# Kernel tuning notes

Hardware: AMD Instinct MI355X
Metric: run time of the kernel (lower is better)

## Reference

```python
import jax, jax.numpy as jnp
import numpy as np

K = 20
EPS = 1e-5
SLOPE = 0.2


def _leaky(v):
    return jnp.where(v >= 0, v, SLOPE * v)


def _instnorm(v, axes):
    # InstanceNorm with affine=False: normalize per (batch, channel) over spatial axes,
    # biased variance, eps=1e-5 (torch default).
    mean = jnp.mean(v, axis=axes, keepdims=True)
    var = jnp.mean((v - mean) ** 2, axis=axes, keepdims=True)
    return (v - mean) * jax.lax.rsqrt(var + EPS)


def _knn_idx(x, k):
    # x: [B, C, N]; returns indices of k nearest neighbors (self included), [B, N, k]
    inner = -2.0 * jnp.einsum('bcn,bcm->bnm', x, x)
    xx = jnp.sum(x * x, axis=1)                      # [B, N]
    pd = -xx[:, :, None] - inner - xx[:, None, :]    # negative squared distance
    return jax.lax.top_k(pd, k)[1]


def _edge_conv(x, w):
    # x: [B, C, N]; w: [O, 2C]. Returns [B, O, N] after max-pool over k neighbors.
    B, C, N = x.shape
    idx = _knn_idx(x, K)                              # [B, N, K]
    xt = jnp.transpose(x, (0, 2, 1))                  # [B, N, C]
    b_idx = jnp.arange(B)[:, None, None]
    nb = xt[b_idx, idx]                               # [B, N, K, C] gathered neighbors
    ctr = xt[:, :, None, :]                           # [B, N, 1, C]
    feat = jnp.concatenate([nb - ctr, jnp.broadcast_to(ctr, nb.shape)], axis=-1)
    h = jnp.einsum('oc,bnkc->bonk', w, feat)          # 1x1 conv as GEMM -> [B, O, N, K]
    h = _leaky(_instnorm(h, (2, 3)))
    return jnp.max(h, axis=-1)                        # [B, O, N]


def setup_inputs() -> dict:
    key = jax.random.key(0)
    ks = jax.random.split(key, 6)
    B, N, feat_dim = 8, 2048, 512
    return {
        'x': jax.random.normal(ks[0], (B, N, 3), dtype=jnp.float32),
        'w1': jax.random.normal(ks[1], (64, 6), dtype=jnp.float32) * 0.1,
        'w2': jax.random.normal(ks[2], (64, 128), dtype=jnp.float32) * 0.1,
        'w3': jax.random.normal(ks[3], (128, 128), dtype=jnp.float32) * 0.1,
        'w4': jax.random.normal(ks[4], (256, 256), dtype=jnp.float32) * 0.1,
        'w5': jax.random.normal(ks[5], (feat_dim, 512), dtype=jnp.float32) * 0.1,
    }


def reference(x, w1, w2, w3, w4, w5):
    xc = jnp.transpose(x, (0, 2, 1))                  # [B, 3, N]
    x1 = _edge_conv(xc, w1)                           # [B, 64, N]
    x2 = _edge_conv(x1, w2)                           # [B, 64, N]
    x3 = _edge_conv(x2, w3)                           # [B, 128, N]
    x4 = _edge_conv(x3, w4)                           # [B, 256, N]
    cat = jnp.concatenate([x1, x2, x3, x4], axis=1)   # [B, 512, N]
    h = jnp.einsum('oc,bcn->bon', w5, cat)            # conv5 (1x1 conv1d)
    feat = _leaky(_instnorm(h, (2,)))
    return feat                                       # [B, feat_dim, N]
```

## Files before the change

kernel.cpp:

```cpp
#include <hip/hip_runtime.h>
#include <math.h>

#define NPTS 2048
#define NB 8
#define KNN 20
#define EPSI 1e-5f
#define SLOPE 0.2f
#define CHUNK 512

__global__ __launch_bounds__(256) void transpose_kernel(const float* __restrict__ xin,
                                                        float* __restrict__ xc) {
    int g = blockIdx.x * 256 + threadIdx.x;
    int b = g / NPTS, n = g % NPTS;
    float v0 = xin[(size_t)g * 3 + 0];
    float v1 = xin[(size_t)g * 3 + 1];
    float v2 = xin[(size_t)g * 3 + 2];
    xc[((size_t)b * 3 + 0) * NPTS + n] = v0;
    xc[((size_t)b * 3 + 1) * NPTS + n] = v1;
    xc[((size_t)b * 3 + 2) * NPTS + n] = v2;
}

__global__ __launch_bounds__(256) void xx_kernel(const float* __restrict__ x, int bstride, int C,
                                                 float* __restrict__ xx) {
    int g = blockIdx.x * 256 + threadIdx.x;
    int b = g / NPTS, n = g % NPTS;
    const float* p = x + (size_t)b * bstride + n;
    float s = 0.f;
    for (int c = 0; c < C; ++c) { float v = p[(size_t)c * NPTS]; s += v * v; }
    xx[g] = s;
}

__global__ __launch_bounds__(256) void pd_gemm(const float* __restrict__ x, int bstride, int C,
                                               const float* __restrict__ xx,
                                               float* __restrict__ pd, int r0) {
    __shared__ float As[16][64];
    __shared__ float Bs[16][64];
    int b = blockIdx.z;
    int nbase_l = blockIdx.y * 64;
    int mbase = blockIdx.x * 64;
    int tx = threadIdx.x, ty = threadIdx.y;
    int tid = ty * 16 + tx;
    float acc[4][4] = {};
    const float* xb = x + (size_t)b * bstride;

    for (int c0 = 0; c0 < C; c0 += 16) {
        int KC = min(16, C - c0);
        for (int t = tid; t < KC * 64; t += 256) {
            int cc = t >> 6, j = t & 63;
            As[cc][j] = xb[(size_t)(c0 + cc) * NPTS + r0 + nbase_l + j];
            Bs[cc][j] = xb[(size_t)(c0 + cc) * NPTS + mbase + j];
        }
        __syncthreads();
        if (KC == 16) {
            #pragma unroll
            for (int cc = 0; cc < 16; ++cc) {
                float a0 = As[cc][ty*4+0], a1 = As[cc][ty*4+1], a2 = As[cc][ty*4+2], a3 = As[cc][ty*4+3];
                float b0 = Bs[cc][tx*4+0], b1 = Bs[cc][tx*4+1], b2 = Bs[cc][tx*4+2], b3 = Bs[cc][tx*4+3];
                acc[0][0] += a0*b0; acc[0][1] += a0*b1; acc[0][2] += a0*b2; acc[0][3] += a0*b3;
                acc[1][0] += a1*b0; acc[1][1] += a1*b1; acc[1][2] += a1*b2; acc[1][3] += a1*b3;
                acc[2][0] += a2*b0; acc[2][1] += a2*b1; acc[2][2] += a2*b2; acc[2][3] += a2*b3;
                acc[3][0] += a3*b0; acc[3][1] += a3*b1; acc[3][2] += a3*b2; acc[3][3] += a3*b3;
            }
        } else {
            for (int cc = 0; cc < KC; ++cc) {
                float a0 = As[cc][ty*4+0], a1 = As[cc][ty*4+1], a2 = As[cc][ty*4+2], a3 = As[cc][ty*4+3];
                float b0 = Bs[cc][tx*4+0], b1 = Bs[cc][tx*4+1], b2 = Bs[cc][tx*4+2], b3 = Bs[cc][tx*4+3];
                acc[0][0] += a0*b0; acc[0][1] += a0*b1; acc[0][2] += a0*b2; acc[0][3] += a0*b3;
                acc[1][0] += a1*b0; acc[1][1] += a1*b1; acc[1][2] += a1*b2; acc[1][3] += a1*b3;
                acc[2][0] += a2*b0; acc[2][1] += a2*b1; acc[2][2] += a2*b2; acc[2][3] += a2*b3;
                acc[3][0] += a3*b0; acc[3][1] += a3*b1; acc[3][2] += a3*b2; acc[3][3] += a3*b3;
            }
        }
        __syncthreads();
    }

    const float* xxb = xx + (size_t)b * NPTS;
    #pragma unroll
    for (int i = 0; i < 4; ++i) {
        int nl = nbase_l + ty * 4 + i;
        float xn = xxb[r0 + nl];
        float4 o;
        o.x = 2.f * acc[i][0] - xn - xxb[mbase + tx*4 + 0];
        o.y = 2.f * acc[i][1] - xn - xxb[mbase + tx*4 + 1];
        o.z = 2.f * acc[i][2] - xn - xxb[mbase + tx*4 + 2];
        o.w = 2.f * acc[i][3] - xn - xxb[mbase + tx*4 + 3];
        *(float4*)&pd[((size_t)b * CHUNK + nl) * NPTS + mbase + tx*4] = o;
    }
}

__global__ __launch_bounds__(256) void topk_kernel(const float* __restrict__ pd,
                                                   int* __restrict__ idxout, int r0) {
    int wid = (blockIdx.x * 256 + threadIdx.x) >> 6;
    int lane = threadIdx.x & 63;
    int b = wid / CHUNK;
    int nl = wid % CHUNK;
    int n = r0 + nl;
    const float* row = pd + ((size_t)b * CHUNK + nl) * NPTS;

    float v[32];
    #pragma unroll
    for (int j = 0; j < 32; ++j) v[j] = row[lane + 64 * j];

    unsigned mask = 0u;
    int saved = 0;
    for (int t = 0; t < KNN; ++t) {
        float best = -INFINITY; int bj = 0;
        #pragma unroll
        for (int j = 0; j < 32; ++j) {
            bool ok = ((mask >> j) & 1u) == 0u;
            if (ok && v[j] > best) { best = v[j]; bj = j; }
        }
        int midx = lane + 64 * bj;
        #pragma unroll
        for (int off = 32; off > 0; off >>= 1) {
            float ov = __shfl_xor(best, off);
            int om = __shfl_xor(midx, off);
            if (ov > best || (ov == best && om < midx)) { best = ov; midx = om; }
        }
        if (lane == t) saved = midx;
        if ((midx & 63) == lane) mask |= 1u << (midx >> 6);
    }
    if (lane < KNN) idxout[((size_t)b * NPTS + n) * KNN + lane] = saved;
}

__global__ __launch_bounds__(256) void yz_gemm(const float* __restrict__ x, int bstride, int C, int O,
                                               const float* __restrict__ w,
                                               float* __restrict__ y, float* __restrict__ z) {
    __shared__ float Xs[128 * 64];
    __shared__ float Ws[4 * 256];
    int b = blockIdx.z;
    int mbase = blockIdx.x * 64;
    int obase = blockIdx.y * 4;
    int tx = threadIdx.x, ty = threadIdx.y;
    int tid = ty * 64 + tx;
    const float* xb = x + (size_t)b * bstride;

    for (int t = tid; t < C * 64; t += 256) {
        int cc = t >> 6, j = t & 63;
        Xs[cc * 64 + j] = xb[(size_t)cc * NPTS + mbase + j];
    }
    int C2 = 2 * C;
    for (int t = tid; t < 4 * C2; t += 256) {
        int ol = t / C2, c = t % C2;
        Ws[ol * C2 + c] = w[(size_t)(obase + ol) * C2 + c];
    }
    __syncthreads();

    int o = obase + ty;
    const float* wr = &Ws[ty * C2];
    float ya = 0.f, za = 0.f;
    for (int c = 0; c < C; ++c) {
        float v = Xs[c * 64 + tx];
        float wd = wr[c], wc = wr[C + c];
        ya += wd * v;
        za += (wc - wd) * v;
    }
    y[((size_t)b * O + o) * NPTS + mbase + tx] = ya;
    z[((size_t)b * O + o) * NPTS + mbase + tx] = za;
}

__global__ __launch_bounds__(256) void gather_norm(const float* __restrict__ y,
                                                   const float* __restrict__ z,
                                                   const int* __restrict__ idx,
                                                   float* __restrict__ cat, int coff, int O) {
    __shared__ float yrow[NPTS];
    __shared__ float red[8];
    int o = blockIdx.x, b = blockIdx.y;
    int tid = threadIdx.x;
    const float* yr = y + ((size_t)b * O + o) * NPTS;
    for (int i = tid; i < NPTS / 4; i += 256)
        ((float4*)yrow)[i] = ((const float4*)yr)[i];
    __syncthreads();

    const float* zr = z + ((size_t)b * O + o) * NPTS;
    float s1 = 0.f, s2 = 0.f;
    float hm[8];
    #pragma unroll
    for (int r = 0; r < 8; ++r) {
        int n = r * 256 + tid;
        float zv = zr[n];
        const int* ip = idx + ((size_t)b * NPTS + n) * KNN;
        float mx = -INFINITY;
        #pragma unroll
        for (int k = 0; k < KNN; ++k) {
            float h = yrow[ip[k]] + zv;
            s1 += h; s2 += h * h;
            mx = fmaxf(mx, h);
        }
        hm[r] = mx;
    }
    #pragma unroll
    for (int off = 32; off > 0; off >>= 1) {
        s1 += __shfl_xor(s1, off);
        s2 += __shfl_xor(s2, off);
    }
    int wv = tid >> 6, lane = tid & 63;
    if (lane == 0) { red[wv] = s1; red[4 + wv] = s2; }
    __syncthreads();
    float S1 = red[0] + red[1] + red[2] + red[3];
    float S2 = red[4] + red[5] + red[6] + red[7];
    const float inv = 1.f / (float)(NPTS * KNN);
    float mean = S1 * inv;
    float var = S2 * inv - mean * mean;
    float rs = 1.f / sqrtf(var + EPSI);
    float* dst = cat + ((size_t)b * 512 + coff + o) * NPTS;
    #pragma unroll
    for (int r = 0; r < 8; ++r) {
        float vv = (hm[r] - mean) * rs;
        dst[r * 256 + tid] = vv >= 0.f ? vv : SLOPE * vv;
    }
}

__global__ __launch_bounds__(256) void final_gemm(const float* __restrict__ w5,
                                                  const float* __restrict__ cat,
                                                  float* __restrict__ h) {
    __shared__ float Wsh[64 * 17];
    __shared__ float Csh[16 * 64];
    int b = blockIdx.z;
    int obase = blockIdx.y * 64, nbase = blockIdx.x * 64;
    int tx = threadIdx.x, ty = threadIdx.y;
    int tid = ty * 16 + tx;
    float acc[4][4] = {};

    for (int c0 = 0; c0 < 512; c0 += 16) {
        for (int t = tid; t < 1024; t += 256) {
            int ol = t >> 4, cc = t & 15;
            Wsh[ol * 17 + cc] = w5[(size_t)(obase + ol) * 512 + c0 + cc];
        }
        for (int t = tid; t < 1024; t += 256) {
            int cc = t >> 6, j = t & 63;
            Csh[cc * 64 + j] = cat[((size_t)b * 512 + c0 + cc) * NPTS + nbase + j];
        }
        __syncthreads();
        #pragma unroll
        for (int cc = 0; cc < 16; ++cc) {
            float a0 = Wsh[(ty*4+0)*17 + cc], a1 = Wsh[(ty*4+1)*17 + cc];
            float a2 = Wsh[(ty*4+2)*17 + cc], a3 = Wsh[(ty*4+3)*17 + cc];
            float b0 = Csh[cc*64 + tx*4+0], b1 = Csh[cc*64 + tx*4+1];
            float b2 = Csh[cc*64 + tx*4+2], b3 = Csh[cc*64 + tx*4+3];
            acc[0][0] += a0*b0; acc[0][1] += a0*b1; acc[0][2] += a0*b2; acc[0][3] += a0*b3;
            acc[1][0] += a1*b0; acc[1][1] += a1*b1; acc[1][2] += a1*b2; acc[1][3] += a1*b3;
            acc[2][0] += a2*b0; acc[2][1] += a2*b1; acc[2][2] += a2*b2; acc[2][3] += a2*b3;
            acc[3][0] += a3*b0; acc[3][1] += a3*b1; acc[3][2] += a3*b2; acc[3][3] += a3*b3;
        }
        __syncthreads();
    }
    #pragma unroll
    for (int i = 0; i < 4; ++i) {
        float4 o4 = make_float4(acc[i][0], acc[i][1], acc[i][2], acc[i][3]);
        *(float4*)&h[((size_t)b * 512 + obase + ty*4 + i) * NPTS + nbase + tx*4] = o4;
    }
}

__global__ __launch_bounds__(256) void final_norm(const float* __restrict__ h,
                                                  float* __restrict__ out) {
    __shared__ float red[8];
    int o = blockIdx.x, b = blockIdx.y;
    int tid = threadIdx.x;
    const float* hr = h + ((size_t)b * 512 + o) * NPTS;
    float s1 = 0.f, s2 = 0.f;
    float v[8];
    #pragma unroll
    for (int r = 0; r < 8; ++r) {
        v[r] = hr[r * 256 + tid];
        s1 += v[r]; s2 += v[r] * v[r];
    }
    #pragma unroll
    for (int off = 32; off > 0; off >>= 1) {
        s1 += __shfl_xor(s1, off);
        s2 += __shfl_xor(s2, off);
    }
    int wv = tid >> 6, lane = tid & 63;
    if (lane == 0) { red[wv] = s1; red[4 + wv] = s2; }
    __syncthreads();
    float S1 = red[0] + red[1] + red[2] + red[3];
    float S2 = red[4] + red[5] + red[6] + red[7];
    const float inv = 1.f / (float)NPTS;
    float mean = S1 * inv;
    float var = S2 * inv - mean * mean;
    float rs = 1.f / sqrtf(var + EPSI);
    float* dst = out + ((size_t)b * 512 + o) * NPTS;
    #pragma unroll
    for (int r = 0; r < 8; ++r) {
        float vv = (v[r] - mean) * rs;
        dst[r * 256 + tid] = vv >= 0.f ? vv : SLOPE * vv;
    }
}

extern "C" void kernel_launch(void* const* d_in, const int* in_sizes, int n_in,
                              void* d_out, int out_size, void* d_ws, size_t ws_size,
                              hipStream_t stream) {
    const float* x_in = (const float*)d_in[0];
    const float* w1 = (const float*)d_in[1];
    const float* w2 = (const float*)d_in[2];
    const float* w3 = (const float*)d_in[3];
    const float* w4 = (const float*)d_in[4];
    const float* w5 = (const float*)d_in[5];
    float* out = (float*)d_out;
    float* ws = (float*)d_ws;

    float* region = ws;
    float* yb = region;
    float* zb = region + 4194304;
    float* pdb = region;
    float* hb = region;
    int* idxb = (int*)(ws + 8388608);
    float* xxb = ws + 8388608 + 327680;
    float* xcb = xxb + NB * NPTS;
    float* cat = xcb + NB * 3 * NPTS;

    transpose_kernel<<<NB * NPTS / 256, 256, 0, stream>>>(x_in, xcb);

    const float* srcs[4] = {xcb, cat, cat + (size_t)64 * NPTS, cat + (size_t)128 * NPTS};
    int bstr[4] = {3 * NPTS, 512 * NPTS, 512 * NPTS, 512 * NPTS};
    int Cin[4] = {3, 64, 64, 128};
    int Oc[4] = {64, 64, 128, 256};
    const float* wl[4] = {w1, w2, w3, w4};
    int coffs[4] = {0, 64, 128, 256};

    for (int li = 0; li < 4; ++li) {
        xx_kernel<<<NB * NPTS / 256, 256, 0, stream>>>(srcs[li], bstr[li], Cin[li], xxb);
        for (int r0 = 0; r0 < NPTS; r0 += CHUNK) {
            pd_gemm<<<dim3(NPTS / 64, CHUNK / 64, NB), dim3(16, 16), 0, stream>>>(
                srcs[li], bstr[li], Cin[li], xxb, pdb, r0);
            topk_kernel<<<NB * CHUNK / 4, 256, 0, stream>>>(pdb, idxb, r0);
        }
        yz_gemm<<<dim3(NPTS / 64, Oc[li] / 4, NB), dim3(64, 4), 0, stream>>>(
            srcs[li], bstr[li], Cin[li], Oc[li], wl[li], yb, zb);
        gather_norm<<<dim3(Oc[li], NB), 256, 0, stream>>>(yb, zb, idxb, cat, coffs[li], Oc[li]);
    }

    final_gemm<<<dim3(NPTS / 64, 8, NB), dim3(16, 16), 0, stream>>>(w5, cat, hb);
    final_norm<<<dim3(512, NB), 256, 0, stream>>>(hb, out);
}
```

Before: 1.594 ms.

## Use split-bf16 MFMA for final GEMM and larger 128x128 tiles for distance GEMM

```diff
diff --git a/kernel.cpp b/kernel.cpp
--- a/kernel.cpp
+++ b/kernel.cpp
@@ -7,6 +7,18 @@
 #define EPSI 1e-5f
 #define SLOPE 0.2f
 #define CHUNK 512
+
+typedef short bf16x8 __attribute__((ext_vector_type(8)));
+typedef float f32x4 __attribute__((ext_vector_type(4)));
+
+__device__ __forceinline__ unsigned short f2bf(float x) {
+    union { float f; unsigned u; } v; v.f = x;
+    unsigned r = v.u + 0x7FFF + ((v.u >> 16) & 1u);
+    return (unsigned short)(r >> 16);
+}
+__device__ __forceinline__ float bf2f(unsigned short h) {
+    union { unsigned u; float f; } v; v.u = ((unsigned)h) << 16; return v.f;
+}
 
 __global__ __launch_bounds__(256) void transpose_kernel(const float* __restrict__ xin,
                                                         float* __restrict__ xc) {
@@ -30,61 +42,64 @@
     xx[g] = s;
 }
 
-__global__ __launch_bounds__(256) void pd_gemm(const float* __restrict__ x, int bstride, int C,
-                                               const float* __restrict__ xx,
-                                               float* __restrict__ pd, int r0) {
-    __shared__ float As[16][64];
-    __shared__ float Bs[16][64];
+__global__ __launch_bounds__(256) void pd_gemm2(const float* __restrict__ x, int bstride, int C,
+                                                const float* __restrict__ xx,
+                                                float* __restrict__ pd, int r0) {
+    __shared__ float As[16][128];
+    __shared__ float Bs[16][128];
     int b = blockIdx.z;
-    int nbase_l = blockIdx.y * 64;
-    int mbase = blockIdx.x * 64;
-    int tx = threadIdx.x, ty = threadIdx.y;
-    int tid = ty * 16 + tx;
-    float acc[4][4] = {};
+    int nbase_l = blockIdx.y * 128;
+    int mbase = blockIdx.x * 128;
+    int tx = threadIdx.x & 15, ty = threadIdx.x >> 4;
+    int tid = threadIdx.x;
+    float acc[8][8] = {};
     const float* xb = x + (size_t)b * bstride;
 
     for (int c0 = 0; c0 < C; c0 += 16) {
         int KC = min(16, C - c0);
-        for (int t = tid; t < KC * 64; t += 256) {
-            int cc = t >> 6, j = t & 63;
-            As[cc][j] = xb[(size_t)(c0 + cc) * NPTS + r0 + nbase_l + j];
-            Bs[cc][j] = xb[(size_t)(c0 + cc) * NPTS + mbase + j];
+        for (int t = tid; t < 512; t += 256) {
+            int cc = t >> 5, j4 = (t & 31) * 4;
+            float4 av = make_float4(0.f, 0.f, 0.f, 0.f), bv = av;
+            if (cc < KC) {
+                av = *(const float4*)&xb[(size_t)(c0 + cc) * NPTS + r0 + nbase_l + j4];
+                bv = *(const float4*)&xb[(size_t)(c0 + cc) * NPTS + mbase + j4];
+            }
+            *(float4*)&As[cc][j4] = av;
+            *(float4*)&Bs[cc][j4] = bv;
         }
         __syncthreads();
-        if (KC == 16) {
+        #pragma unroll
+        for (int cc = 0; cc < 16; ++cc) {
+            float av[8], bv[8];
+            *(float4*)&av[0] = *(float4*)&As[cc][ty * 8];
+            *(float4*)&av[4] = *(float4*)&As[cc][ty * 8 + 4];
+            *(float4*)&bv[0] = *(float4*)&Bs[cc][tx * 8];
+            *(float4*)&bv[4] = *(float4*)&Bs[cc][tx * 8 + 4];
             #pragma unroll
-            for (int cc = 0; cc < 16; ++cc) {
-                float a0 = As[cc][ty*4+0], a1 = As[cc][ty*4+1], a2 = As[cc][ty*4+2], a3 = As[cc][ty*4+3];
-                float b0 = Bs[cc][tx*4+0], b1 = Bs[cc][tx*4+1], b2 = Bs[cc][tx*4+2], b3 = Bs[cc][tx*4+3];
-                acc[0][0] += a0*b0; acc[0][1] += a0*b1; acc[0][2] += a0*b2; acc[0][3] += a0*b3;
-                acc[1][0] += a1*b0; acc[1][1] += a1*b1; acc[1][2] += a1*b2; acc[1][3] += a1*b3;
-                acc[2][0] += a2*b0; acc[2][1] += a2*b1; acc[2][2] += a2*b2; acc[2][3] += a2*b3;
-                acc[3][0] += a3*b0; acc[3][1] += a3*b1; acc[3][2] += a3*b2; acc[3][3] += a3*b3;
-            }
-        } else {
-            for (int cc = 0; cc < KC; ++cc) {
-                float a0 = As[cc][ty*4+0], a1 = As[cc][ty*4+1], a2 = As[cc][ty*4+2], a3 = As[cc][ty*4+3];
-                float b0 = Bs[cc][tx*4+0], b1 = Bs[cc][tx*4+1], b2 = Bs[cc][tx*4+2], b3 = Bs[cc][tx*4+3];
-                acc[0][0] += a0*b0; acc[0][1] += a0*b1; acc[0][2] += a0*b2; acc[0][3] += a0*b3;
-                acc[1][0] += a1*b0; acc[1][1] += a1*b1; acc[1][2] += a1*b2; acc[1][3] += a1*b3;
-                acc[2][0] += a2*b0; acc[2][1] += a2*b1; acc[2][2] += a2*b2; acc[2][3] += a2*b3;
-                acc[3][0] += a3*b0; acc[3][1] += a3*b1; acc[3][2] += a3*b2; acc[3][3] += a3*b3;
-            }
+            for (int i = 0; i < 8; ++i)
+                #pragma unroll
+                for (int j = 0; j < 8; ++j)
+                    acc[i][j] += av[i] * bv[j];
         }
         __syncthreads();
     }
 
     const float* xxb = xx + (size_t)b * NPTS;
     #pragma unroll
-    for (int i = 0; i < 4; ++i) {
-        int nl = nbase_l + ty * 4 + i;
+    for (int i = 0; i < 8; ++i) {
+        int nl = nbase_l + ty * 8 + i;
         float xn = xxb[r0 + nl];
-        float4 o;
-        o.x = 2.f * acc[i][0] - xn - xxb[mbase + tx*4 + 0];
-        o.y = 2.f * acc[i][1] - xn - xxb[mbase + tx*4 + 1];
-        o.z = 2.f * acc[i][2] - xn - xxb[mbase + tx*4 + 2];
-        o.w = 2.f * acc[i][3] - xn - xxb[mbase + tx*4 + 3];
-        *(float4*)&pd[((size_t)b * CHUNK + nl) * NPTS + mbase + tx*4] = o;
+        float4 o0, o1;
+        o0.x = 2.f * acc[i][0] - xn - xxb[mbase + tx*8 + 0];
+        o0.y = 2.f * acc[i][1] - xn - xxb[mbase + tx*8 + 1];
+        o0.z = 2.f * acc[i][2] - xn - xxb[mbase + tx*8 + 2];
+        o0.w = 2.f * acc[i][3] - xn - xxb[mbase + tx*8 + 3];
+        o1.x = 2.f * acc[i][4] - xn - xxb[mbase + tx*8 + 4];
+        o1.y = 2.f * acc[i][5] - xn - xxb[mbase + tx*8 + 5];
+        o1.z = 2.f * acc[i][6] - xn - xxb[mbase + tx*8 + 6];
+        o1.w = 2.f * acc[i][7] - xn - xxb[mbase + tx*8 + 7];
+        *(float4*)&pd[((size_t)b * CHUNK + nl) * NPTS + mbase + tx*8] = o0;
+        *(float4*)&pd[((size_t)b * CHUNK + nl) * NPTS + mbase + tx*8 + 4] = o1;
     }
 }
 
@@ -131,8 +146,8 @@
     int b = blockIdx.z;
     int mbase = blockIdx.x * 64;
     int obase = blockIdx.y * 4;
-    int tx = threadIdx.x, ty = threadIdx.y;
-    int tid = ty * 64 + tx;
+    int tx = threadIdx.x & 63, ty = threadIdx.x >> 6;
+    int tid = threadIdx.x;
     const float* xb = x + (size_t)b * bstride;
 
     for (int t = tid; t < C * 64; t += 256) {
@@ -211,45 +226,88 @@
     }
 }
 
-__global__ __launch_bounds__(256) void final_gemm(const float* __restrict__ w5,
-                                                  const float* __restrict__ cat,
-                                                  float* __restrict__ h) {
-    __shared__ float Wsh[64 * 17];
-    __shared__ float Csh[16 * 64];
+__global__ __launch_bounds__(256) void w5_prep(const float* __restrict__ w5,
+                                               unsigned short* __restrict__ wh,
+                                               unsigned short* __restrict__ wl) {
+    int i = blockIdx.x * 256 + threadIdx.x;
+    float x = w5[i];
+    unsigned short h = f2bf(x);
+    wh[i] = h;
+    wl[i] = f2bf(x - bf2f(h));
+}
+
+__global__ __launch_bounds__(256) void catT_prep(const float* __restrict__ cat,
+                                                 unsigned short* __restrict__ cth,
+                                                 unsigned short* __restrict__ ctl) {
+    __shared__ float t[32][33];
     int b = blockIdx.z;
-    int obase = blockIdx.y * 64, nbase = blockIdx.x * 64;
-    int tx = threadIdx.x, ty = threadIdx.y;
-    int tid = ty * 16 + tx;
-    float acc[4][4] = {};
-
-    for (int c0 = 0; c0 < 512; c0 += 16) {
-        for (int t = tid; t < 1024; t += 256) {
-            int ol = t >> 4, cc = t & 15;
-            Wsh[ol * 17 + cc] = w5[(size_t)(obase + ol) * 512 + c0 + cc];
-        }
-        for (int t = tid; t < 1024; t += 256) {
-            int cc = t >> 6, j = t & 63;
-            Csh[cc * 64 + j] = cat[((size_t)b * 512 + c0 + cc) * NPTS + nbase + j];
-        }
-        __syncthreads();
-        #pragma unroll
-        for (int cc = 0; cc < 16; ++cc) {
-            float a0 = Wsh[(ty*4+0)*17 + cc], a1 = Wsh[(ty*4+1)*17 + cc];
-            float a2 = Wsh[(ty*4+2)*17 + cc], a3 = Wsh[(ty*4+3)*17 + cc];
-            float b0 = Csh[cc*64 + tx*4+0], b1 = Csh[cc*64 + tx*4+1];
-            float b2 = Csh[cc*64 + tx*4+2], b3 = Csh[cc*64 + tx*4+3];
-            acc[0][0] += a0*b0; acc[0][1] += a0*b1; acc[0][2] += a0*b2; acc[0][3] += a0*b3;
-            acc[1][0] += a1*b0; acc[1][1] += a1*b1; acc[1][2] += a1*b2; acc[1][3] += a1*b3;
-            acc[2][0] += a2*b0; acc[2][1] += a2*b1; acc[2][2] += a2*b2; acc[2][3] += a2*b3;
-            acc[3][0] += a3*b0; acc[3][1] += a3*b1; acc[3][2] += a3*b2; acc[3][3] += a3*b3;
-        }
-        __syncthreads();
-    }
-    #pragma unroll
-    for (int i = 0; i < 4; ++i) {
-        float4 o4 = make_float4(acc[i][0], acc[i][1], acc[i][2], acc[i][3]);
-        *(float4*)&h[((size_t)b * 512 + obase + ty*4 + i) * NPTS + nbase + tx*4] = o4;
-    }
+    int n0 = blockIdx.x * 32, c0 = blockIdx.y * 32;
+    int tx = threadIdx.x & 31, ty = threadIdx.x >> 5;
+    #pragma unroll
+    for (int r = 0; r < 4; ++r) {
+        int ci = ty + r * 8;
+        t[ci][tx] = cat[((size_t)b * 512 + c0 + ci) * NPTS + n0 + tx];
+    }
+    __syncthreads();
+    #pragma unroll
+    for (int r = 0; r < 4; ++r) {
+        int ni = ty + r * 8;
+        float x = t[tx][ni];
+        unsigned short h = f2bf(x);
+        size_t off = ((size_t)b * NPTS + n0 + ni) * 512 + c0 + tx;
+        cth[off] = h;
+        ctl[off] = f2bf(x - bf2f(h));
+    }
+}
+
+__global__ __launch_bounds__(256) void final_gemm_mfma(const unsigned short* __restrict__ wh,
+                                                       const unsigned short* __restrict__ wl,
+                                                       const unsigned short* __restrict__ cth,
+                                                       const unsigned short* __restrict__ ctl,
+                                                       float* __restrict__ h) {
+    int b = blockIdx.z;
+    int nbase = blockIdx.x * 64, obase = blockIdx.y * 64;
+    int w = threadIdx.x >> 6, l = threadIdx.x & 63;
+    int wr = (w >> 1) * 32, wc = (w & 1) * 32;
+    int lr = l & 15, lk = (l >> 4) * 8;
+
+    f32x4 acc[2][2] = {};
+    const unsigned short* aH = wh + (size_t)(obase + wr + lr) * 512 + lk;
+    const unsigned short* aL = wl + (size_t)(obase + wr + lr) * 512 + lk;
+    const unsigned short* bH = cth + ((size_t)b * NPTS + nbase + wc + lr) * 512 + lk;
+    const unsigned short* bL = ctl + ((size_t)b * NPTS + nbase + wc + lr) * 512 + lk;
+
+    for (int k0 = 0; k0 < 512; k0 += 32) {
+        bf16x8 ah[2], al[2], bh[2], bl[2];
+        #pragma unroll
+        for (int mi = 0; mi < 2; ++mi) {
+            ah[mi] = *(const bf16x8*)(aH + (size_t)mi * 16 * 512 + k0);
+            al[mi] = *(const bf16x8*)(aL + (size_t)mi * 16 * 512 + k0);
+        }
+        #pragma unroll
+        for (int ni = 0; ni < 2; ++ni) {
+            bh[ni] = *(const bf16x8*)(bH + (size_t)ni * 16 * 512 + k0);
+            bl[ni] = *(const bf16x8*)(bL + (size_t)ni * 16 * 512 + k0);
+        }
+        #pragma unroll
+        for (int mi = 0; mi < 2; ++mi)
+            #pragma unroll
+            for (int ni = 0; ni < 2; ++ni) {
+                acc[mi][ni] = __builtin_amdgcn_mfma_f32_16x16x32_bf16(ah[mi], bh[ni], acc[mi][ni], 0, 0, 0);
+                acc[mi][ni] = __builtin_amdgcn_mfma_f32_16x16x32_bf16(ah[mi], bl[ni], acc[mi][ni], 0, 0, 0);
+                acc[mi][ni] = __builtin_amdgcn_mfma_f32_16x16x32_bf16(al[mi], bh[ni], acc[mi][ni], 0, 0, 0);
+            }
+    }
+
+    int orow = obase + wr + (l >> 4) * 4;
+    int ncol = nbase + wc + lr;
+    #pragma unroll
+    for (int mi = 0; mi < 2; ++mi)
+        #pragma unroll
+        for (int r = 0; r < 4; ++r)
+            #pragma unroll
+            for (int ni = 0; ni < 2; ++ni)
+                h[((size_t)b * 512 + orow + mi * 16 + r) * NPTS + ncol + ni * 16] = acc[mi][ni][r];
 }
 
 __global__ __launch_bounds__(256) void final_norm(const float* __restrict__ h,
@@ -303,13 +361,18 @@
     float* yb = region;
     float* zb = region + 4194304;
     float* pdb = region;
-    float* hb = region;
     int* idxb = (int*)(ws + 8388608);
     float* xxb = ws + 8388608 + 327680;
     float* xcb = xxb + NB * NPTS;
     float* cat = xcb + NB * 3 * NPTS;
+    unsigned short* w5h = (unsigned short*)(cat + 8388608);
+    unsigned short* w5l = w5h + 262144;
+    unsigned short* cth = (unsigned short*)region;
+    unsigned short* ctl = cth + (size_t)NB * NPTS * 512;
+    float* hb = cat;
 
     transpose_kernel<<<NB * NPTS / 256, 256, 0, stream>>>(x_in, xcb);
+    w5_prep<<<512 * 512 / 256, 256, 0, stream>>>(w5, w5h, w5l);
 
     const float* srcs[4] = {xcb, cat, cat + (size_t)64 * NPTS, cat + (size_t)128 * NPTS};
     int bstr[4] = {3 * NPTS, 512 * NPTS, 512 * NPTS, 512 * NPTS};
@@ -321,15 +384,16 @@
     for (int li = 0; li < 4; ++li) {
         xx_kernel<<<NB * NPTS / 256, 256, 0, stream>>>(srcs[li], bstr[li], Cin[li], xxb);
         for (int r0 = 0; r0 < NPTS; r0 += CHUNK) {
-            pd_gemm<<<dim3(NPTS / 64, CHUNK / 64, NB), dim3(16, 16), 0, stream>>>(
+            pd_gemm2<<<dim3(NPTS / 128, CHUNK / 128, NB), 256, 0, stream>>>(
                 srcs[li], bstr[li], Cin[li], xxb, pdb, r0);
             topk_kernel<<<NB * CHUNK / 4, 256, 0, stream>>>(pdb, idxb, r0);
         }
-        yz_gemm<<<dim3(NPTS / 64, Oc[li] / 4, NB), dim3(64, 4), 0, stream>>>(
+        yz_gemm<<<dim3(NPTS / 64, Oc[li] / 4, NB), dim3(256), 0, stream>>>(
             srcs[li], bstr[li], Cin[li], Oc[li], wl[li], yb, zb);
         gather_norm<<<dim3(Oc[li], NB), 256, 0, stream>>>(yb, zb, idxb, cat, coffs[li], Oc[li]);
     }
 
-    final_gemm<<<dim3(NPTS / 64, 8, NB), dim3(16, 16), 0, stream>>>(w5, cat, hb);
+    catT_prep<<<dim3(NPTS / 32, 512 / 32, NB), 256, 0, stream>>>(cat, cth, ctl);
+    final_gemm_mfma<<<dim3(NPTS / 64, 512 / 64, NB), 256, 0, stream>>>(w5h, w5l, cth, ctl, hb);
     final_norm<<<dim3(512, NB), 256, 0, stream>>>(hb, out);
 }
```

After: 1.530 ms. 4.1% less time.
